# Kernel optimization log

Measured on AMD Instinct MI355X. Metric: run time of the kernel, lower is better.

Reference implementation:

```python
import jax, jax.numpy as jnp
import numpy as np

U, L, B = 512, 512, 256  # units, num_layers (rectangular mesh: L == U), batch
PI = float(np.pi)


def cc_mul(a, b):
    # complex multiply of stacked (real, imag) tensors
    return jnp.stack((a[0] * b[0] - a[1] * b[1], a[0] * b[1] + a[1] * b[0]))


def i_mul(c):
    # s_mul(1j, c): multiply stacked complex by 1j -> (-im, re)
    return jnp.stack((-c[1], c[0]))


def setup_inputs() -> dict:
    key = jax.random.key(0)
    ks = jax.random.split(key, 8)
    x = jax.random.normal(ks[0], (2, B, U), jnp.float32)
    two_pi = 2.0 * PI
    theta = jax.random.uniform(ks[1], (L, U // 2), jnp.float32) * two_pi
    phi = jax.random.uniform(ks[2], (L, U // 2), jnp.float32) * two_pi
    gamma = jax.random.uniform(ks[3], (U,), jnp.float32) * two_pi
    mask = jnp.ones((L, U // 2), jnp.float32)
    enn = jax.random.uniform(ks[4], (U, L), jnp.float32)
    enp = jax.random.uniform(ks[5], (U, L), jnp.float32)
    epn = jax.random.uniform(ks[6], (U, L), jnp.float32)
    epp = jax.random.uniform(ks[7], (U, L), jnp.float32)
    # rectangular-mesh permutations: identity at input/output, interior layers
    # alternate circular shifts so MZIs couple (0,1),(2,3),... then (1,2),(3,4),...
    perms = np.tile(np.arange(U, dtype=np.int32), (L + 1, 1))
    for l in range(1, L):
        perms[l] = np.roll(perms[l], 1 if l % 2 else -1)
    perms = jnp.asarray(perms)
    # pairwise off-diagonal permutation: swap adjacent pairs [1,0,3,2,...]
    pairwise_perm = jnp.asarray(
        np.arange(U, dtype=np.int32).reshape(-1, 2)[:, ::-1].ravel())
    return dict(x=x, theta=theta, phi=phi, gamma=gamma, mask=mask,
                enn=enn, enp=enp, epn=epn, epp=epp,
                perms=perms, pairwise_perm=pairwise_perm)


def reference(x, theta, phi, gamma, mask, enn, enp, epn, epp, perms, pairwise_perm):
    # --- MeshPhasesTorch (basis='sm', hadamard=False) ---
    inv = 1.0 - mask
    th = theta * mask + inv * PI  # (1 - hadamard) * pi
    ph = phi * mask + inv * PI

    def stripe(p):  # single_mode_arrangement: [L, U//2] -> [U, L]
        return jnp.zeros((U, L), p.dtype).at[::2].set(p.T)

    internal = stripe(th)
    external = stripe(ph)
    ipsl = jnp.stack((jnp.cos(internal), jnp.sin(internal)))  # [2, U, L]
    epsl = jnp.stack((jnp.cos(external), jnp.sin(external)))  # [2, U, L]

    roll_m1 = lambda t: jnp.roll(t, -1, axis=1)  # along units axis
    roll_p1 = lambda t: jnp.roll(t, 1, axis=1)

    # --- MeshTorch.mesh_layers (hadamard=False branch) ---
    s11 = epp * ipsl - enn * roll_m1(ipsl)
    s22 = roll_p1(-enn * ipsl + epp * roll_m1(ipsl))
    s12 = i_mul(roll_p1(enp * ipsl + epn * roll_m1(ipsl)))
    s21 = i_mul(epn * ipsl + enp * roll_m1(ipsl))

    diag = cc_mul(epsl, s11 + s22) * 0.5              # [2, U, L]
    off = cc_mul(roll_p1(epsl), s21 + s12) * 0.5      # [2, U, L]
    diag = jnp.transpose(diag, (0, 2, 1))             # [2, L, U]
    off = jnp.transpose(off, (0, 2, 1))

    # --- forward: input phase shift, then sequential vertical layers ---
    in_ps = jnp.stack((jnp.cos(gamma), jnp.sin(gamma)))  # [2, U]
    out = cc_mul(x, in_ps[:, None, :])                   # [2, B, U]
    out = out[..., perms[0]]                             # left perm of layer 0

    def step(carry, inp):
        d, o, rp = inp  # [2, U], [2, U], [U]
        y = cc_mul(carry, d[:, None, :]) \
            + cc_mul(carry, o[:, None, :])[..., pairwise_perm]
        return y[..., rp], None

    xs = (jnp.moveaxis(diag, 1, 0), jnp.moveaxis(off, 1, 0), perms[1:])
    out, _ = jax.lax.scan(step, out, xs)
    return out
```

## Files before the change

kernel.cpp:

```cpp
#include <hip/hip_runtime.h>
#include <hip/hip_fp16.h>


#define UU 512
#define LL 512
#define BB 256
#define KK 256
#define KF 4
#define N9 128
#define W9 9
#define N17 64
#define W17 17
#define N33 32
#define W33 33


__global__ __launch_bounds__(512, 2) void mesh_build4(
    const float* __restrict__ theta, const float* __restrict__ phi,
    const float* __restrict__ enn,   const float* __restrict__ enp,
    const float* __restrict__ epn,   const float* __restrict__ epp,
    float2* __restrict__ g9)
{
    __shared__ float2 gwj[7 * UU];
    __shared__ float2 xbuf[2][UU];
    const int u  = threadIdx.x;
    const int j  = ((blockIdx.x & 7) << 4) | (blockIdx.x >> 3);
    const int um = (u + UU - 1) & (UU - 1);
    const int l0 = j * KF;

    const float4 epp_u4 = *(const float4*)(epp + u * LL + l0);
    const float4 epp_m4 = *(const float4*)(epp + um * LL + l0);
    const float4 enn_u4 = *(const float4*)(enn + u * LL + l0);
    const float4 enn_m4 = *(const float4*)(enn + um * LL + l0);
    const float4 enp_u4 = *(const float4*)(enp + u * LL + l0);
    const float4 enp_m4 = *(const float4*)(enp + um * LL + l0);
    const float4 epn_u4 = *(const float4*)(epn + u * LL + l0);
    const float4 epn_m4 = *(const float4*)(epn + um * LL + l0);
    const float epp_u8[4] = {epp_u4.x, epp_u4.y, epp_u4.z, epp_u4.w};
    const float epp_m8[4] = {epp_m4.x, epp_m4.y, epp_m4.z, epp_m4.w};
    const float enn_u8[4] = {enn_u4.x, enn_u4.y, enn_u4.z, enn_u4.w};
    const float enn_m8[4] = {enn_m4.x, enn_m4.y, enn_m4.z, enn_m4.w};
    const float enp_u8[4] = {enp_u4.x, enp_u4.y, enp_u4.z, enp_u4.w};
    const float enp_m8[4] = {enp_m4.x, enp_m4.y, enp_m4.z, enp_m4.w};
    const float epn_u8[4] = {epn_u4.x, epn_u4.y, epn_u4.z, epn_u4.w};
    const float epn_m8[4] = {epn_m4.x, epn_m4.y, epn_m4.z, epn_m4.w};

    const int ka = u >> 1;
    const int kb = ((u + 1) >> 1) & (KK - 1);
    float thA[KF], thB[KF], phC[KF];
    #pragma unroll
    for (int s = 0; s < KF; ++s) {
        thA[s] = theta[(l0 + s) * KK + ka];
        thB[s] = theta[(l0 + s) * KK + kb];
        phC[s] = phi  [(l0 + s) * KK + ka];
    }

    const bool uodd = (u & 1) != 0;

    #define COEF(s, DR, DI, OR_, OI_) { \
        float sA, cA, sB, cB, sC, cC; \
        __sincosf(thA[s], &sA, &cA); \
        __sincosf(thB[s], &sB, &cB); \
        __sincosf(phC[s], &sC, &cC); \
        const float ipu_r = uodd ? 1.f : cA, ipu_i = uodd ? 0.f : sA; \
        const float ipp_r = uodd ? cB : 1.f, ipp_i = uodd ? sB : 0.f; \
        const float ipm_r = uodd ? cA : 1.f, ipm_i = uodd ? sA : 0.f; \
        const float epu_r = uodd ? 1.f : cC, epu_i = uodd ? 0.f : sC; \
        const float epm_r = uodd ? cC : 1.f, epm_i = uodd ? sC : 0.f; \
        const float sd_r = epp_u8[s]*ipu_r - enn_u8[s]*ipp_r - enn_m8[s]*ipm_r + epp_m8[s]*ipu_r; \
        const float sd_i = epp_u8[s]*ipu_i - enn_u8[s]*ipp_i - enn_m8[s]*ipm_i + epp_m8[s]*ipu_i; \
        DR = 0.5f * (epu_r * sd_r - epu_i * sd_i); \
        DI = 0.5f * (epu_r * sd_i + epu_i * sd_r); \
        const float so_r = epn_u8[s]*ipu_r + enp_u8[s]*ipp_r + enp_m8[s]*ipm_r + epn_m8[s]*ipu_r; \
        const float so_i = epn_u8[s]*ipu_i + enp_u8[s]*ipp_i + enp_m8[s]*ipm_i + epn_m8[s]*ipu_i; \
        const float soi_r = -so_i, soi_i = so_r; \
        OR_ = 0.5f * (epm_r * soi_r - epm_i * soi_i); \
        OI_ = 0.5f * (epm_r * soi_i + epm_i * soi_r); }

    float dcur_r, dcur_i, o0_r, o0_i;
    COEF(0, dcur_r, dcur_i, o0_r, o0_i)
    gwj[u] = make_float2(1.f, 0.f);
    xbuf[0][u] = make_float2(o0_r, o0_i);
    __syncthreads();

    int sigma = 0;
    const int tb = uodd ? 0 : 2;
    float2 outr[W9];

    #pragma unroll
    for (int s = 0; s < KF; ++s) {
        const int W  = 2 * s + 1;
        const int Wn = W + 2;
        const int a  = (u + sigma) & (UU - 1);
        const int bx = ((u ^ 1) + sigma) & (UU - 1);
        const float2 ox = xbuf[s & 1][u ^ 1];
        const float dr = dcur_r, di = dcur_i, orr = ox.x, oi = ox.y;

        #pragma unroll
        for (int tn = 0; tn < W9; ++tn) {
            float ar = 0.f, ai = 0.f;
            if (tn < Wn) {
                const int tp = tn - 1;
                const int ts = tn - tb;
                if (0 <= tp && tp < W) {
                    float2 gv = gwj[tp * UU + a];
                    ar += dr * gv.x - di * gv.y;
                    ai += dr * gv.y + di * gv.x;
                }
                if (0 <= ts && ts < W) {
                    float2 gv = gwj[ts * UU + bx];
                    ar += orr * gv.x - oi * gv.y;
                    ai += orr * gv.y + oi * gv.x;
                }
            }
            outr[tn] = make_float2(ar, ai);
        }

        if (s < KF - 1) {
            float dn_r, dn_i, on_r, on_i;
            COEF(s + 1, dn_r, dn_i, on_r, on_i)
            __syncthreads();
            const int wd = (u + sigma) & (UU - 1);
            #pragma unroll
            for (int tn = 0; tn < W9; ++tn)
                if (tn < Wn) gwj[tn * UU + wd] = outr[tn];
            xbuf[(s + 1) & 1][u] = make_float2(on_r, on_i);
            dcur_r = dn_r; dcur_i = dn_i;
            sigma += (s & 1) ? 1 : -1;
            __syncthreads();
        }
    }
    #undef COEF

    const int v = (j == N9 - 1) ? u : um;
    #pragma unroll
    for (int t = 0; t < W9; ++t)
        g9[(j * W9 + t) * UU + v] = outr[t];
}

__global__ __launch_bounds__(512, 2) void mesh_merge33(
    const float2* __restrict__ g9, __half2* __restrict__ g2h)
{
    __shared__ float2 A1[W17 * 80];
    __shared__ float2 A2[W17 * 64];
    const int tid = threadIdx.x;
    const int q   = blockIdx.x & 31;
    const int c   = blockIdx.x >> 5;
    const int u0  = c << 6;
    const int loA2  = (q == N33 - 1) ? -5 : -4;
    const int loC   = (q == N33 - 1) ? -9 : -8;
    const int kbase = u0 + loC;

    const float2* __restrict__ g9a = g9 + (4 * q    ) * W9 * UU;
    const float2* __restrict__ g9b = g9 + (4 * q + 1) * W9 * UU;
    const float2* __restrict__ g9c = g9 + (4 * q + 2) * W9 * UU;
    const float2* __restrict__ g9d = g9 + (4 * q + 3) * W9 * UU;

    for (int e = tid; e < W17 * 80; e += 512) {
        const int tb = e / 80;
        const int kk = e - tb * 80;
        const int k  = (kbase + kk + UU) & (UU - 1);
        float ar = 0.f, ai = 0.f;
        #pragma unroll
        for (int a = 0; a < W9; ++a) {
            const int tbm = tb - a;
            if (0 <= tbm && tbm < W9) {
                const float2 va = g9b[a * UU + k];
                const float2 vb = g9a[tbm * UU + ((k - 4 + a + UU) & (UU - 1))];
                ar += va.x * vb.x - va.y * vb.y;
                ai += va.x * vb.y + va.y * vb.x;
            }
        }
        A1[e] = make_float2(ar, ai);
    }

    for (int e = tid; e < W17 * 64; e += 512) {
        const int ta = e >> 6;
        const int uu = e & 63;
        const int u  = u0 + uu;
        float ar = 0.f, ai = 0.f;
        #pragma unroll
        for (int a = 0; a < W9; ++a) {
            const int tam = ta - a;
            if (0 <= tam && tam < W9) {
                const float2 va = g9d[a * UU + u];
                const float2 vb = g9c[tam * UU + ((u + loA2 + a + UU) & (UU - 1))];
                ar += va.x * vb.x - va.y * vb.y;
                ai += va.x * vb.y + va.y * vb.x;
            }
        }
        A2[e] = make_float2(ar, ai);
    }
    __syncthreads();

    for (int e = tid; e < W33 * 64; e += 512) {
        const int t  = e >> 6;
        const int uu = e & 63;
        float ar = 0.f, ai = 0.f;
        #pragma unroll
        for (int ta = 0; ta < W17; ++ta) {
            const int tbm = t - ta;
            if (0 <= tbm && tbm < W17) {
                const float2 va = A2[ta * 64 + uu];
                const float2 vb = A1[tbm * 80 + uu + ta];
                ar += va.x * vb.x - va.y * vb.y;
                ai += va.x * vb.y + va.y * vb.x;
            }
        }
        g2h[(q * W33 + t) * UU + (u0 + uu)] = __floats2half2_rn(ar, ai);
    }
}

__global__ __launch_bounds__(512, 2) void mesh_apply(
    const float* __restrict__ x, const float* __restrict__ gamma,
    const __half2* __restrict__ g2h, float* __restrict__ out)
{
    __shared__ float2 sbuf[2][548];
    const int u = threadIdx.x;
    const int b = blockIdx.x;

    float sg, cg;
    __sincosf(gamma[u], &sg, &cg);
    const float xr = x[b * UU + u];
    const float xi = x[BB * UU + b * UU + u];
    float2 v = make_float2(xr * cg - xi * sg, xr * sg + xi * cg);

    #define STORE_STATE(pp)                                                   \
        do {                                                                  \
            sbuf[pp][u + 17] = v;                                             \
            if (u >= 495) sbuf[pp][u - 495] = v;          \
            if (u < 16)   sbuf[pp][u + 529] = v;          \
        } while (0)

    STORE_STATE(0);

    float2 gg[W33];
    {
        const __half2* gq = g2h + u;
        #pragma unroll
        for (int t = 0; t < W33; ++t) gg[t] = __half22float2(gq[t * UU]);
    }
    __syncthreads();

    for (int q = 0; q < N33; ++q) {
        const int p = q & 1;
        const int base = u + ((q == N33 - 1) ? 0 : 1);

        float2 w[W33];
        #pragma unroll
        for (int t = 0; t < W33; ++t) w[t] = sbuf[p][base + t];

        float ar = 0.f, ai = 0.f;
        #pragma unroll
        for (int t = 0; t < W33; ++t) {
            ar += gg[t].x * w[t].x - gg[t].y * w[t].y;
            ai += gg[t].x * w[t].y + gg[t].y * w[t].x;
        }
        v = make_float2(ar, ai);

        if (q < N33 - 1) {
            const __half2* gq = g2h + (q + 1) * (W33 * UU) + u;
            #pragma unroll
            for (int t = 0; t < W33; ++t) gg[t] = __half22float2(gq[t * UU]);
            STORE_STATE(1 - p);
            __syncthreads();
        }
    }

    out[b * UU + u]           = v.x;
    out[BB * UU + b * UU + u] = v.y;
    #undef STORE_STATE
}

#define RSLOTS 6
#define WAITVM40() __builtin_amdgcn_s_waitcnt(0x8F78)
#define STAGE(gg, ss)                                                        \
    _Pragma("unroll")                                                        \
    for (int jq = 0; jq < 8; ++jq)                                           \
        __builtin_amdgcn_global_load_lds(                                    \
            (const __attribute__((address_space(1))) void*)(coef + (gg) * UU + jq * 64 + lane), \
            (__attribute__((address_space(3))) void*)&ring[(ss) * UU + jq * 64], \
            16, 0, 0);

__global__ __launch_bounds__(512) void mesh_precompute_slot(
    const float* __restrict__ theta, const float* __restrict__ phi,
    const float* __restrict__ enn,   const float* __restrict__ enp,
    const float* __restrict__ epn,   const float* __restrict__ epp,
    float4* __restrict__ coef)
{
    const int u  = threadIdx.x;
    const int l  = blockIdx.x;
    const int um = (u + UU - 1) & (UU - 1);
    const float epp_u  = epp[u * LL + l],  epp_um = epp[um * LL + l];
    const float enn_u  = enn[u * LL + l],  enn_um = enn[um * LL + l];
    const float enp_u  = enp[u * LL + l],  enp_um = enp[um * LL + l];
    const float epn_u  = epn[u * LL + l],  epn_um = epn[um * LL + l];
    float ipu_r, ipu_i, ipp_r, ipp_i, ipm_r, ipm_i;
    float epu_r, epu_i, epm_r, epm_i;
    if ((u & 1) == 0) {
        const int k = u >> 1;
        float th = theta[l * KK + k];  __sincosf(th, &ipu_i, &ipu_r);
        ipp_r = 1.f; ipp_i = 0.f;  ipm_r = 1.f; ipm_i = 0.f;
        float phv = phi[l * KK + k];   __sincosf(phv, &epu_i, &epu_r);
        epm_r = 1.f; epm_i = 0.f;
    } else {
        ipu_r = 1.f; ipu_i = 0.f;
        float thp = theta[l * KK + (((u + 1) >> 1) & (KK - 1))]; __sincosf(thp, &ipp_i, &ipp_r);
        float thm = theta[l * KK + (u >> 1)];                    __sincosf(thm, &ipm_i, &ipm_r);
        epu_r = 1.f; epu_i = 0.f;
        float phm = phi[l * KK + (u >> 1)];                      __sincosf(phm, &epm_i, &epm_r);
    }
    const float sd_r = epp_u * ipu_r - enn_u * ipp_r - enn_um * ipm_r + epp_um * ipu_r;
    const float sd_i = epp_u * ipu_i - enn_u * ipp_i - enn_um * ipm_i + epp_um * ipu_i;
    const float d_r = 0.5f * (epu_r * sd_r - epu_i * sd_i);
    const float d_i = 0.5f * (epu_r * sd_i + epu_i * sd_r);
    const float so_r = epn_u * ipu_r + enp_u * ipp_r + enp_um * ipm_r + epn_um * ipu_r;
    const float so_i = epn_u * ipu_i + enp_u * ipp_i + enp_um * ipm_i + epn_um * ipu_i;
    const float soi_r = -so_i, soi_i = so_r;
    const float o_r = 0.5f * (epm_r * soi_r - epm_i * soi_i);
    const float o_i = 0.5f * (epm_r * soi_i + epm_i * soi_r);
    const int slot = ((u & 7) << 6) | (u >> 3);
    coef[l * UU + slot] = make_float4(d_r, d_i, o_r, o_i);
}

#define PAIR_MIX(K)                                                         \
    _Pragma("unroll")                                                       \
    for (int p = 0; p < 4; ++p) {                                           \
        const float4 ke = K[2*p], ko = K[2*p+1];                            \
        y0r[p] = c0r[p]*ke.x - c0i[p]*ke.y + c1r[p]*ko.z - c1i[p]*ko.w;     \
        y0i[p] = c0r[p]*ke.y + c0i[p]*ke.x + c1r[p]*ko.w + c1i[p]*ko.z;     \
        y1r[p] = c1r[p]*ko.x - c1i[p]*ko.y + c0r[p]*ke.z - c0i[p]*ke.w;     \
        y1i[p] = c1r[p]*ko.y + c1i[p]*ko.x + c0r[p]*ke.w + c0i[p]*ke.z;     \
    }

__global__ __launch_bounds__(64) void mesh_chain_r3(
    const float* __restrict__ x, const float* __restrict__ gamma,
    const float4* __restrict__ coef, float* __restrict__ out)
{
    __shared__ float4 ring[RSLOTS * UU];
    const int lane = threadIdx.x;
    const int b    = blockIdx.x;
    const int m0   = lane << 3;
    #pragma unroll
    for (int pl = 0; pl < RSLOTS; ++pl) { STAGE(pl, pl) }
    const float4 xr0 = *(const float4*)(x + b * UU + m0);
    const float4 xr1 = *(const float4*)(x + b * UU + m0 + 4);
    const float4 xi0 = *(const float4*)(x + BB * UU + b * UU + m0);
    const float4 xi1 = *(const float4*)(x + BB * UU + b * UU + m0 + 4);
    const float xr[8] = {xr0.x, xr0.y, xr0.z, xr0.w, xr1.x, xr1.y, xr1.z, xr1.w};
    const float xi[8] = {xi0.x, xi0.y, xi0.z, xi0.w, xi1.x, xi1.y, xi1.z, xi1.w};
    float c0r[4], c0i[4], c1r[4], c1i[4];
    #pragma unroll
    for (int p = 0; p < 4; ++p) {
        float s0, cg0, s1, cg1;
        __sincosf(gamma[m0 + 2*p],     &s0, &cg0);
        __sincosf(gamma[m0 + 2*p + 1], &s1, &cg1);
        c0r[p] = xr[2*p] * cg0 - xi[2*p] * s0;
        c0i[p] = xr[2*p] * s0  + xi[2*p] * cg0;
        c1r[p] = xr[2*p+1] * cg1 - xi[2*p+1] * s1;
        c1i[p] = xr[2*p+1] * s1  + xi[2*p+1] * cg1;
    }
    const int laneM1 = (lane + 63) & 63;
    const int laneP1 = (lane + 1) & 63;
    int sa = 0;
    for (int it = 0; it < 256; ++it) {
        float y0r[4], y0i[4], y1r[4], y1i[4];
        WAITVM40();
        float4 k[8];
        #pragma unroll
        for (int q = 0; q < 8; ++q) k[q] = ring[sa * UU + q * 64 + lane];
        PAIR_MIX(k)
        {
            const float br = __shfl(y1r[3], laneM1, 64);
            const float bi = __shfl(y1i[3], laneM1, 64);
            #pragma unroll
            for (int p = 3; p > 0; --p) { c0r[p] = y1r[p-1]; c0i[p] = y1i[p-1]; }
            c0r[0] = br; c0i[0] = bi;
            #pragma unroll
            for (int p = 0; p < 4; ++p) { c1r[p] = y0r[p]; c1i[p] = y0i[p]; }
        }
        { const int g1 = (2 * it + RSLOTS) & (LL - 1); STAGE(g1, sa) }
        WAITVM40();
        float4 n[8];
        #pragma unroll
        for (int q = 0; q < 8; ++q) n[q] = ring[(sa + 1) * UU + q * 64 + lane];
        PAIR_MIX(n)
        if (it < 255) {
            const float br = __shfl(y0r[0], laneP1, 64);
            const float bi = __shfl(y0i[0], laneP1, 64);
            #pragma unroll
            for (int p = 0; p < 3; ++p) { c0r[p] = y1r[p]; c0i[p] = y1i[p];
                                          c1r[p] = y0r[p+1]; c1i[p] = y0i[p+1]; }
            c0r[3] = y1r[3]; c0i[3] = y1i[3];
            c1r[3] = br;     c1i[3] = bi;
        } else {
            #pragma unroll
            for (int p = 0; p < 4; ++p) { c0r[p] = y0r[p]; c0i[p] = y0i[p];
                                          c1r[p] = y1r[p]; c1i[p] = y1i[p]; }
        }
        { const int g2 = (2 * it + RSLOTS + 1) & (LL - 1); STAGE(g2, sa + 1) }
        sa += 2; if (sa >= RSLOTS) sa = 0;
    }
    *(float4*)(out + b * UU + m0)               = make_float4(c0r[0], c1r[0], c0r[1], c1r[1]);
    *(float4*)(out + b * UU + m0 + 4)           = make_float4(c0r[2], c1r[2], c0r[3], c1r[3]);
    *(float4*)(out + BB * UU + b * UU + m0)     = make_float4(c0i[0], c1i[0], c0i[1], c1i[1]);
    *(float4*)(out + BB * UU + b * UU + m0 + 4) = make_float4(c0i[2], c1i[2], c0i[3], c1i[3]);
}

extern "C" void kernel_launch(void* const* d_in, const int* in_sizes, int n_in,
                              void* d_out, int out_size, void* d_ws, size_t ws_size,
                              hipStream_t stream) {
    (void)in_sizes; (void)n_in; (void)out_size;
    const float* x     = (const float*)d_in[0];
    const float* theta = (const float*)d_in[1];
    const float* phi   = (const float*)d_in[2];
    const float* gamma = (const float*)d_in[3];
    const float* enn   = (const float*)d_in[5];
    const float* enp   = (const float*)d_in[6];
    const float* epn   = (const float*)d_in[7];
    const float* epp   = (const float*)d_in[8];
    float* out = (float*)d_out;

    if (ws_size >= (size_t)6881280) {
        float2*  g9  = (float2*)d_ws;
        __half2* g2h = (__half2*)((char*)d_ws + 4718592);

        mesh_build4<<<N9, UU, 0, stream>>>(theta, phi, enn, enp, epn, epp, g9);
        mesh_merge33<<<N33 * 8, UU, 0, stream>>>(g9, g2h);
        mesh_apply<<<BB, UU, 0, stream>>>(x, gamma, g2h, out);
    } else {
        float4* coef = (float4*)d_ws;
        mesh_precompute_slot<<<LL, UU, 0, stream>>>(theta, phi, enn, enp, epn, epp, coef);
        mesh_chain_r3<<<BB, 64, 0, stream>>>(x, gamma, coef, out);
    }
}
```

Measured before the change: 144.3 us.

## Repack fp16 coefficients into 16-byte blocks and double-buffer loads in mesh_apply

The builder now writes each 33-tap coefficient group in an interleaved layout, so four consecutive taps per unit sit in one 16-byte word plus a scalar tail. mesh_apply loads the next group with 8 wide vector loads plus one scalar, double-buffered across two register sets, and issues those loads before the current step's math. The barrier is replaced by a custom one that waits only on LDS counters, so the global prefetch can stay in flight across it. Split FMA accumulators shorten dependency chains. The risks are higher register pressure and reliance on the hand-written wait count for correctness.

```diff
diff --git a/kernel.cpp b/kernel.cpp
--- a/kernel.cpp
+++ b/kernel.cpp
@@ -13,6 +13,9 @@
 #define W17 17
 #define N33 32
 #define W33 33
+#define GQSTRIDE 67584
+#define GBLK     8192
+#define GTAIL    65536
 
 
 __global__ __launch_bounds__(512, 2) void mesh_build4(
@@ -193,21 +196,27 @@
     }
     __syncthreads();
 
-    for (int e = tid; e < W33 * 64; e += 512) {
-        const int t  = e >> 6;
-        const int uu = e & 63;
-        float ar = 0.f, ai = 0.f;
-        #pragma unroll
-        for (int ta = 0; ta < W17; ++ta) {
-            const int tbm = t - ta;
-            if (0 <= tbm && tbm < W17) {
-                const float2 va = A2[ta * 64 + uu];
-                const float2 vb = A1[tbm * 80 + uu + ta];
-                ar += va.x * vb.x - va.y * vb.y;
-                ai += va.x * vb.y + va.y * vb.x;
+    {
+        __half2* __restrict__ gq = g2h + q * (W33 * UU);
+        for (int e = tid; e < W33 * 64; e += 512) {
+            const int t  = e >> 6;
+            const int uu = e & 63;
+            float ar = 0.f, ai = 0.f;
+            #pragma unroll
+            for (int ta = 0; ta < W17; ++ta) {
+                const int tbm = t - ta;
+                if (0 <= tbm && tbm < W17) {
+                    const float2 va = A2[ta * 64 + uu];
+                    const float2 vb = A1[tbm * 80 + uu + ta];
+                    ar += va.x * vb.x - va.y * vb.y;
+                    ai += va.x * vb.y + va.y * vb.x;
+                }
             }
-        }
-        g2h[(q * W33 + t) * UU + (u0 + uu)] = __floats2half2_rn(ar, ai);
+            const int u = u0 + uu;
+            const int idx = (t < 32) ? ((t >> 2) * 2048 + u * 4 + (t & 3))
+                                     : (16384 + u);
+            gq[idx] = __floats2half2_rn(ar, ai);
+        }
     }
 }
 
@@ -232,43 +241,79 @@
             if (u < 16)   sbuf[pp][u + 529] = v;          \
         } while (0)
 
+    #define BARRIER()                                                         \
+        do {                                                                  \
+            asm volatile("s_waitcnt lgkmcnt(0)" ::: "memory");                \
+            __builtin_amdgcn_s_barrier();                                     \
+            asm volatile("" ::: "memory");                                    \
+        } while (0)
+
+    const char* __restrict__ gb = (const char*)g2h;
+    const int offBlk = u * 16;
+    const int offTl  = GTAIL + u * 4;
+
+    uint4 GA[8]; uint GA32;
+    uint4 GB[8]; uint GB32;
+    #define LOADG(DST, DST32, PL)                                             \
+        do {                                                                  \
+            _Pragma("unroll")                                                 \
+            for (int bq = 0; bq < 8; ++bq)                                    \
+                DST[bq] = *(const uint4*)((PL) + bq * GBLK + offBlk);         \
+            DST32 = *(const uint*)((PL) + offTl);                             \
+        } while (0)
+
+    LOADG(GA, GA32, gb);
     STORE_STATE(0);
-
-    float2 gg[W33];
-    {
-        const __half2* gq = g2h + u;
-        #pragma unroll
-        for (int t = 0; t < W33; ++t) gg[t] = __half22float2(gq[t * UU]);
-    }
-    __syncthreads();
-
-    for (int q = 0; q < N33; ++q) {
-        const int p = q & 1;
-        const int base = u + ((q == N33 - 1) ? 0 : 1);
-
-        float2 w[W33];
-        #pragma unroll
-        for (int t = 0; t < W33; ++t) w[t] = sbuf[p][base + t];
-
-        float ar = 0.f, ai = 0.f;
-        #pragma unroll
-        for (int t = 0; t < W33; ++t) {
-            ar += gg[t].x * w[t].x - gg[t].y * w[t].y;
-            ai += gg[t].x * w[t].y + gg[t].y * w[t].x;
-        }
-        v = make_float2(ar, ai);
-
-        if (q < N33 - 1) {
-            const __half2* gq = g2h + (q + 1) * (W33 * UU) + u;
-            #pragma unroll
-            for (int t = 0; t < W33; ++t) gg[t] = __half22float2(gq[t * UU]);
-            STORE_STATE(1 - p);
-            __syncthreads();
-        }
+    BARRIER();
+
+    #define STEP(QV, CUR, CUR32, NXT, NXT32)                                  \
+    {                                                                         \
+        const int q = (QV);                                                   \
+        if (q < N33 - 1) LOADG(NXT, NXT32, gb + (q + 1) * GQSTRIDE);          \
+        const int p    = q & 1;                                               \
+        const int base = u + ((q == N33 - 1) ? 0 : 1);                        \
+        float ar0 = 0.f, ai0 = 0.f, ar1 = 0.f, ai1 = 0.f;                     \
+        _Pragma("unroll")                                                     \
+        for (int bq = 0; bq < 8; ++bq) {                                      \
+            const uint wd[4] = {CUR[bq].x, CUR[bq].y, CUR[bq].z, CUR[bq].w};  \
+            _Pragma("unroll")                                                 \
+            for (int i = 0; i < 4; ++i) {                                     \
+                const __half2 h = *(const __half2*)&wd[i];                    \
+                const float gx = __half2float(__low2half(h));                 \
+                const float gy = __half2float(__high2half(h));                \
+                const float2 wv = sbuf[p][base + 4 * bq + i];                 \
+                if ((i & 1) == 0) {                                           \
+                    ar0 = fmaf(gx, wv.x, ar0);  ar0 = fmaf(-gy, wv.y, ar0);   \
+                    ai0 = fmaf(gx, wv.y, ai0);  ai0 = fmaf(gy, wv.x, ai0);    \
+                } else {                                                      \
+                    ar1 = fmaf(gx, wv.x, ar1);  ar1 = fmaf(-gy, wv.y, ar1);   \
+                    ai1 = fmaf(gx, wv.y, ai1);  ai1 = fmaf(gy, wv.x, ai1);    \
+                }                                                             \
+            }                                                                 \
+        }                                                                     \
+        {                                                         \
+            const __half2 h = *(const __half2*)&CUR32;                        \
+            const float gx = __half2float(__low2half(h));                     \
+            const float gy = __half2float(__high2half(h));                    \
+            const float2 wv = sbuf[p][base + 32];                             \
+            ar0 = fmaf(gx, wv.x, ar0);  ar0 = fmaf(-gy, wv.y, ar0);           \
+            ai0 = fmaf(gx, wv.y, ai0);  ai0 = fmaf(gy, wv.x, ai0);            \
+        }                                                                     \
+        v = make_float2(ar0 + ar1, ai0 + ai1);                                \
+        if (q < N33 - 1) { STORE_STATE(1 - p); BARRIER(); }                   \
+    }
+
+    #pragma unroll 1
+    for (int it = 0; it < N33 / 2; ++it) {
+        STEP(2 * it,     GA, GA32, GB, GB32)
+        STEP(2 * it + 1, GB, GB32, GA, GA32)
     }
 
     out[b * UU + u]           = v.x;
     out[BB * UU + b * UU + u] = v.y;
+    #undef STEP
+    #undef LOADG
+    #undef BARRIER
     #undef STORE_STATE
 }
 
```

Result: faster. 136.7 us (-5.2%).
